# Performance work log

Hardware: AMD Instinct MI355X
Metric: run time of the kernel (lower is better)

Reference implementation:

```python
import jax, jax.numpy as jnp
import numpy as np
from jax import lax

H = 100  # hidden size hard-coded in the module


def setup_inputs() -> dict:
    key = jax.random.key(0)
    ks = jax.random.split(key, 13)
    T = 8192
    s = 1.0 / np.sqrt(H)  # torch LSTMCell/Linear init scale
    f32 = jnp.float32
    return {
        "input": jax.random.normal(ks[0], (T, 1), f32),
        "encoder_state_h": jax.random.normal(ks[1], (1, H), f32),
        "encoder_state_c": jax.random.normal(ks[2], (1, H), f32),
        "w_ih1": jax.random.normal(ks[3], (4 * H, 1), f32) * s,
        "w_hh1": jax.random.normal(ks[4], (4 * H, H), f32) * s,
        "b_ih1": jax.random.normal(ks[5], (4 * H,), f32) * s,
        "b_hh1": jax.random.normal(ks[6], (4 * H,), f32) * s,
        "w_ih2": jax.random.normal(ks[7], (4 * H, H), f32) * s,
        "w_hh2": jax.random.normal(ks[8], (4 * H, H), f32) * s,
        "b_ih2": jax.random.normal(ks[9], (4 * H,), f32) * s,
        "b_hh2": jax.random.normal(ks[10], (4 * H,), f32) * s,
        "w_lin": jax.random.normal(ks[11], (1, H), f32) * s,
        "b_lin": jax.random.normal(ks[12], (1,), f32) * s,
        "future": 1024,
    }


def _lstm_cell(x, h, c, w_ih, w_hh, b_ih, b_hh):
    # torch.nn.LSTMCell: gates ordered i, f, g, o
    gates = x @ w_ih.T + h @ w_hh.T + b_ih + b_hh  # (1, 4H)
    i, f, g, o = jnp.split(gates, 4, axis=-1)
    c_new = jax.nn.sigmoid(f) * c + jax.nn.sigmoid(i) * jnp.tanh(g)
    h_new = jax.nn.sigmoid(o) * jnp.tanh(c_new)
    return h_new, c_new


def reference(input, encoder_state_h, encoder_state_c,
              w_ih1, w_hh1, b_ih1, b_hh1,
              w_ih2, w_hh2, b_ih2, b_hh2,
              w_lin, b_lin, future):
    dt = input.dtype

    def step(carry, x_t):
        h1, c1, h2, c2 = carry
        h1, c1 = _lstm_cell(x_t, h1, c1, w_ih1, w_hh1, b_ih1, b_hh1)
        h2, c2 = _lstm_cell(h1, h2, c2, w_ih2, w_hh2, b_ih2, b_hh2)
        y = h2 @ w_lin.T + b_lin  # (1, 1)
        return (h1, c1, h2, c2), y

    carry0 = (encoder_state_h, encoder_state_c,
              jnp.zeros((1, H), dt), jnp.zeros((1, H), dt))
    xs = input[:, None, :]  # (T, 1, 1): per-step (1,1) input as in chunk(dim=0)
    carry, ys = lax.scan(step, carry0, xs)
    seq_out = ys[:, 0, 0][None, :]  # (1, T)

    if future:
        def fstep(carry, _):
            h1, c1, h2, c2, y = carry
            h1, c1 = _lstm_cell(y, h1, c1, w_ih1, w_hh1, b_ih1, b_hh1)
            h2, c2 = _lstm_cell(h1, h2, c2, w_ih2, w_hh2, b_ih2, b_hh2)
            y = h2 @ w_lin.T + b_lin
            return (h1, c1, h2, c2, y), y

        fcarry0 = carry + (ys[-1],)
        _, fys = lax.scan(fstep, fcarry0, None, length=future)
        fut_out = fys[:, 0, 0][None, :]  # (1, future)
        return jnp.concatenate([seq_out, fut_out], axis=1)  # (1, T+future)
    return seq_out
```

## Files before the change

### kernel.cpp

```cpp
#include <hip/hip_runtime.h>
#include <math.h>


#define HH 100
#define NT 512
#define ROWS 400
#define SPIN_CAP 2000000u

#define OFF_AW     0
#define OFF_P2W    128
#define OFF_BPROG  256
#define OFF_YPROG  384
#define OFF_YSLOT  512
#define OFF_RING   16384

#define VMCNT0() asm volatile("s_waitcnt vmcnt(0)" ::: "memory")
#define VMCNT2() asm volatile("s_waitcnt vmcnt(2)" ::: "memory")
#define LGKM0()  asm volatile("s_waitcnt lgkmcnt(0)" ::: "memory")
#define CLOB()   asm volatile("" ::: "memory")

__device__ __forceinline__ float rl(float v, int k) {
    return __int_as_float(__builtin_amdgcn_readlane(__float_as_int(v), k));
}
__device__ __forceinline__ unsigned san(unsigned v) { return v > 0x00FFFFFFu ? 0u : v; }
__device__ __forceinline__ unsigned ldu(const unsigned* p) {
    return san(__hip_atomic_load((unsigned*)p, __ATOMIC_RELAXED, __HIP_MEMORY_SCOPE_AGENT));
}
__device__ __forceinline__ void stu(unsigned* p, unsigned v) {
    __hip_atomic_store(p, v, __ATOMIC_RELAXED, __HIP_MEMORY_SCOPE_AGENT);
}
__device__ __forceinline__ float ld_f(const float* p) {
    return __hip_atomic_load((float*)p, __ATOMIC_RELAXED, __HIP_MEMORY_SCOPE_AGENT);
}
__device__ __forceinline__ void st_wt(float* p, float v) {
    __hip_atomic_store(p, v, __ATOMIC_RELAXED, __HIP_MEMORY_SCOPE_AGENT);
}
__device__ __forceinline__ void wait_ge(unsigned* p, unsigned need, unsigned& cache) {
    if (cache >= need) return;
    unsigned s = 0;
    do { cache = ldu(p); } while (cache < need && ++s < SPIN_CAP);
    VMCNT0();
}
__device__ __forceinline__ void wait_min8(unsigned* q, unsigned need, unsigned& cache) {
    if (cache >= need) return;
    unsigned s = 0;
    for (;;) {
        unsigned m0 = ldu(q), m1 = ldu(q + 1), m2 = ldu(q + 2), m3 = ldu(q + 3);
        unsigned m4 = ldu(q + 4), m5 = ldu(q + 5), m6 = ldu(q + 6), m7 = ldu(q + 7);
        unsigned a = m0 < m1 ? m0 : m1, b = m2 < m3 ? m2 : m3;
        unsigned c = m4 < m5 ? m4 : m5, d = m6 < m7 ? m6 : m7;
        a = a < b ? a : b;  c = c < d ? c : d;
        cache = a < c ? a : c;
        if (cache >= need || ++s > SPIN_CAP) break;
    }
    VMCNT0();
}
__device__ __forceinline__ void bar() {
    LGKM0();
    __builtin_amdgcn_s_barrier();
    CLOB();
}
__device__ __forceinline__ float fast_sigm(float x) {
    return __builtin_amdgcn_rcpf(1.0f + __expf(-x));
}
__device__ __forceinline__ float fast_tanh(float x) {
    return fmaf(-2.0f, __builtin_amdgcn_rcpf(1.0f + __expf(2.0f * x)), 1.0f);
}
__device__ __forceinline__ const float4* opqp(const float4* p) {
    unsigned long long u = (unsigned long long)p;
    asm("" : "+v"(u));
    return (const float4*)u;
}

#define REP25(M) M(0) M(1) M(2) M(3) M(4) M(5) M(6) M(7) M(8) M(9) M(10) M(11) \
                 M(12) M(13) M(14) M(15) M(16) M(17) M(18) M(19) M(20) M(21) M(22) M(23) M(24)
#define DECLW(i) float4 W_##i;
#define LOADW(i) W_##i = wrow[i];
#define DOTC(i) { \
    const float hsv = ((i) < 16) ? hv0 : hv1; \
    const int kb = ((i) < 16) ? (4 * (i)) : (4 * ((i) - 16)); \
    float h0 = rl(hsv, kb), h1 = rl(hsv, kb + 1), h2 = rl(hsv, kb + 2), h3 = rl(hsv, kb + 3); \
    a0 = fmaf(W_##i.x, h0, a0); a1 = fmaf(W_##i.y, h1, a1); \
    a0 = fmaf(W_##i.z, h2, a0); a1 = fmaf(W_##i.w, h3, a1); \
}

extern "C" __global__ void __launch_bounds__(NT, 2)
__attribute__((amdgpu_waves_per_eu(2, 2)))
decoder_kernel(const float* __restrict__ input,
               const float* __restrict__ enc_h,
               const float* __restrict__ enc_c,
               const float* __restrict__ w_ih1,
               const float* __restrict__ w_hh1,
               const float* __restrict__ b_ih1,
               const float* __restrict__ b_hh1,
               const float* __restrict__ w_ih2,
               const float* __restrict__ w_hh2,
               const float* __restrict__ b_ih2,
               const float* __restrict__ b_hh2,
               const float* __restrict__ w_lin,
               const float* __restrict__ b_lin,
               float* __restrict__ out,
               char* __restrict__ ws,
               int T, int F, int S)
{
    const int tid = threadIdx.x;
    const int l = tid & 63;
    const int w = tid >> 6;
    unsigned* aw     = (unsigned*)(ws + OFF_AW);
    unsigned* p2w    = (unsigned*)(ws + OFF_P2W);
    unsigned* b_prog = (unsigned*)(ws + OFF_BPROG);
    unsigned* y_prog = (unsigned*)(ws + OFF_YPROG);
    float* y_slot = (float*)(ws + OFF_YSLOT);
    float* ring1  = (float*)(ws + OFF_RING);
    float* ring2  = ring1 + (size_t)S * HH;
    const int smask = S - 1;
    const int TOT = T + F;

    const int cell = 16 * w + (l & 15);
    const int gate = l >> 4;
    const bool valid = (cell < 100);
    const bool c_lane = (gate == 0) && valid;

    if (blockIdx.x == 0) {
        __shared__ __align__(16) float h1s[2][128];
        const int j = valid ? (cell + 100 * gate) : 0;
        const float4* wrow = opqp((const float4*)(w_hh1 + (size_t)j * HH));
        REP25(DECLW)
        REP25(LOADW)
        const float wx = w_ih1[j];
        const float bi = b_ih1[j] + b_hh1[j];
        float cst = c_lane ? enc_c[cell] : 0.f;
        if (tid < 128) {
            h1s[0][tid] = (tid < HH) ? enc_h[tid] : 0.f;
            h1s[1][tid] = 0.f;
        }
        __syncthreads();

        unsigned cp2 = 0, cy = 0;
        for (int t = 0; t < TOT; ++t) {
            VMCNT0();
            if (l == 0 && t > 0) stu(&aw[w], (unsigned)t);
            float x = 0.f;
            if (t < T) x = input[t];
            if (t >= S) wait_min8(p2w, (unsigned)(t - S + 1), cp2);
            float hv0 = h1s[t & 1][l];
            float hv1 = h1s[t & 1][64 + l];
            float a0 = 0.f, a1 = 0.f;
            REP25(DOTC)
            float acc = bi + a0 + a1;
            if (t >= T) {
                wait_ge(y_prog, (unsigned)(t - T + 1), cy);
                x = ld_f(&y_slot[t - T]);
            }
            acc = fmaf(x, wx, acc);
            float v = (gate == 2) ? fast_tanh(acc) : fast_sigm(acc);
            float gf = __shfl(v, (l & 15) + 16);
            float gg = __shfl(v, (l & 15) + 32);
            float go = __shfl(v, (l & 15) + 48);
            if (c_lane) {
                cst = fmaf(gf, cst, v * gg);
                float h = go * fast_tanh(cst);
                h1s[(t + 1) & 1][cell] = h;
                st_wt(&ring1[(size_t)(t & smask) * HH + cell], h);
            }
            bar();
        }
        VMCNT0();
        if (l == 0) stu(&aw[w], (unsigned)TOT);
    } else if (blockIdx.x == 1) {
        const bool av = (tid < ROWS);
        const int j = av ? tid : 0;
        const float4* wrow = opqp((const float4*)(w_ih2 + (size_t)j * HH));
        REP25(DECLW)
        REP25(LOADW)
        const float bi = b_ih2[j] + b_hh2[j];

        unsigned ca = 0, cb = 0;
        wait_min8(aw, 1u, ca);
        float cv0 = ld_f(ring1 + l);
        float cv1 = (l < 36) ? ld_f(ring1 + 64 + l) : 0.f;
        for (int t = 1; t < T; ++t) {
            VMCNT2();
            if (l == 0 && t >= 3) stu(&p2w[w], (unsigned)(t - 2));
            if (t - 1 >= S) wait_ge(b_prog, (unsigned)(t - S), cb);
            wait_min8(aw, (unsigned)(t + 1), ca);
            const float* rp = ring1 + (size_t)(t & smask) * HH;
            float nv0 = ld_f(rp + l);
            float nv1 = (l < 36) ? ld_f(rp + 64 + l) : 0.f;
            float hv0 = cv0, hv1 = cv1;
            float a0 = 0.f, a1 = 0.f;
            REP25(DOTC)
            float* wpp = ring2 + (size_t)((t - 1) & smask) * ROWS;
            if (av) st_wt(wpp + j, bi + a0 + a1);
            cv0 = nv0; cv1 = nv1;
        }
        VMCNT0();
        if (l == 0) stu(&p2w[w], (unsigned)(T - 1));
        {
            if (T - 1 >= S) wait_ge(b_prog, (unsigned)(T - S), cb);
            float hv0 = cv0, hv1 = cv1;
            float a0 = 0.f, a1 = 0.f;
            REP25(DOTC)
            float* wpp = ring2 + (size_t)((T - 1) & smask) * ROWS;
            if (av) st_wt(wpp + j, bi + a0 + a1);
        }
        VMCNT0();
        if (l == 0) stu(&p2w[w], (unsigned)T);
        for (int t = T; t < TOT; ++t) {
            if (t >= S) wait_ge(b_prog, (unsigned)(t - S + 1), cb);
            wait_min8(aw, (unsigned)(t + 1), ca);
            const float* rp = ring1 + (size_t)(t & smask) * HH;
            float hv0 = ld_f(rp + l);
            float hv1 = (l < 36) ? ld_f(rp + 64 + l) : 0.f;
            float a0 = 0.f, a1 = 0.f;
            REP25(DOTC)
            float* wpp = ring2 + (size_t)(t & smask) * ROWS;
            if (av) st_wt(wpp + j, bi + a0 + a1);
            VMCNT0();
            if (l == 0) stu(&p2w[w], (unsigned)(t + 1));
        }
    } else {
        __shared__ __align__(16) float h2s[2][128];
        __shared__ float yw[2][8];
        const int j = valid ? (cell + 100 * gate) : 0;
        const float4* wrow = opqp((const float4*)(w_hh2 + (size_t)j * HH));
        REP25(DECLW)
        REP25(LOADW)
        const float wl = c_lane ? w_lin[cell] : 0.f;
        const float bl = b_lin[0];
        float cst = 0.f;
        if (tid < 128) { h2s[0][tid] = 0.f; h2s[1][tid] = 0.f; }
        __syncthreads();

        unsigned cpB = 0;
        for (int u = 0; u < TOT; ++u) {
            if (tid == 0 && u > 0) {
                const float* yq = yw[(u - 1) & 1];
                float y = yq[0] + yq[1] + yq[2] + yq[3] + yq[4] + yq[5] + yq[6] + bl;
                stu(b_prog, (unsigned)u);
                if (u - 1 >= T - 1) {
                    st_wt(&y_slot[(u - 1) - (T - 1)], y);
                    VMCNT0();
                    stu(y_prog, (unsigned)(u - T + 1));
                }
                out[u - 1] = y;
            }
            float hv0 = h2s[u & 1][l];
            float hv1 = h2s[u & 1][64 + l];
            const float* pp = ring2 + (size_t)(u & smask) * ROWS;
            float pre;
            float a0 = 0.f, a1 = 0.f;
            if (u < T) {
                wait_min8(p2w, (unsigned)(u + 1), cpB);
                pre = ld_f(pp + j);
                REP25(DOTC)
            } else {
                REP25(DOTC)
                wait_min8(p2w, (unsigned)(u + 1), cpB);
                pre = ld_f(pp + j);
            }
            float acc = pre + a0 + a1;
            float v = (gate == 2) ? fast_tanh(acc) : fast_sigm(acc);
            float gf = __shfl(v, (l & 15) + 16);
            float gg = __shfl(v, (l & 15) + 32);
            float go = __shfl(v, (l & 15) + 48);
            float py = 0.f;
            if (c_lane) {
                cst = fmaf(gf, cst, v * gg);
                float h = go * fast_tanh(cst);
                h2s[(u + 1) & 1][cell] = h;
                py = h * wl;
            }
            py += __shfl_down(py, 8);
            py += __shfl_down(py, 4);
            py += __shfl_down(py, 2);
            py += __shfl_down(py, 1);
            if (l == 0 && w < 7) yw[u & 1][w] = py;
            bar();
        }
        if (tid == 0) {
            const float* yq = yw[(TOT - 1) & 1];
            out[TOT - 1] = yq[0] + yq[1] + yq[2] + yq[3] + yq[4] + yq[5] + yq[6] + bl;
        }
    }
}

extern "C" void kernel_launch(void* const* d_in, const int* in_sizes, int n_in,
                              void* d_out, int out_size, void* d_ws, size_t ws_size,
                              hipStream_t stream) {
    const float* input = (const float*)d_in[0];
    const float* enc_h = (const float*)d_in[1];
    const float* enc_c = (const float*)d_in[2];
    const float* w_ih1 = (const float*)d_in[3];
    const float* w_hh1 = (const float*)d_in[4];
    const float* b_ih1 = (const float*)d_in[5];
    const float* b_hh1 = (const float*)d_in[6];
    const float* w_ih2 = (const float*)d_in[7];
    const float* w_hh2 = (const float*)d_in[8];
    const float* b_ih2 = (const float*)d_in[9];
    const float* b_hh2 = (const float*)d_in[10];
    const float* w_lin = (const float*)d_in[11];
    const float* b_lin = (const float*)d_in[12];
    (void)n_in;

    int T = in_sizes[0];
    int F = out_size - T;
    if (F < 0) F = 0;

    int S = 16;
    while ((size_t)OFF_RING + (size_t)S * 2 * (HH + ROWS) * 4 <= ws_size && S < 8192)
        S <<= 1;

    decoder_kernel<<<dim3(3), dim3(NT), 0, stream>>>(
        input, enc_h, enc_c, w_ih1, w_hh1, b_ih1, b_hh1,
        w_ih2, w_hh2, b_ih2, b_hh2, w_lin, b_lin,
        (float*)d_out, (char*)d_ws, T, F, S);
}
```

Baseline: 16.83 ms.

## Move recurrent weights from registers to LDS plus per-step global reads

Recurrent weights were held in registers. Each block now stages the first 36 columns of its weight matrix into dynamic shared memory at startup and reads the remaining 64 columns from global memory on every timestep. The register-pinning asm trick and the waves-per-EU hint are removed. This lowers register pressure, but it puts LDS and global (L1/L2) loads on the serial recurrence's critical path every step.

After: 29.87 ms. 1.78x slower.

```diff
diff --git a/kernel.cpp b/kernel.cpp
--- a/kernel.cpp
+++ b/kernel.cpp
@@ -5,6 +5,8 @@
 #define HH 100
 #define NT 512
 #define ROWS 400
+#define LCH 9
+#define LDW (LCH * 4)
 #define SPIN_CAP 2000000u
 
 #define OFF_AW     0
@@ -18,6 +20,8 @@
 #define VMCNT2() asm volatile("s_waitcnt vmcnt(2)" ::: "memory")
 #define LGKM0()  asm volatile("s_waitcnt lgkmcnt(0)" ::: "memory")
 #define CLOB()   asm volatile("" ::: "memory")
+
+extern __shared__ __attribute__((aligned(16))) float ldsW[];
 
 __device__ __forceinline__ float rl(float v, int k) {
     return __int_as_float(__builtin_amdgcn_readlane(__float_as_int(v), k));
@@ -66,26 +70,23 @@
 __device__ __forceinline__ float fast_tanh(float x) {
     return fmaf(-2.0f, __builtin_amdgcn_rcpf(1.0f + __expf(2.0f * x)), 1.0f);
 }
-__device__ __forceinline__ const float4* opqp(const float4* p) {
-    unsigned long long u = (unsigned long long)p;
-    asm("" : "+v"(u));
-    return (const float4*)u;
-}
-
-#define REP25(M) M(0) M(1) M(2) M(3) M(4) M(5) M(6) M(7) M(8) M(9) M(10) M(11) \
-                 M(12) M(13) M(14) M(15) M(16) M(17) M(18) M(19) M(20) M(21) M(22) M(23) M(24)
-#define DECLW(i) float4 W_##i;
-#define LOADW(i) W_##i = wrow[i];
-#define DOTC(i) { \
+
+#define DOTS(i, P) { \
     const float hsv = ((i) < 16) ? hv0 : hv1; \
     const int kb = ((i) < 16) ? (4 * (i)) : (4 * ((i) - 16)); \
+    float4 Wc = P[(i) < LCH ? (i) : ((i) - 0)]; \
     float h0 = rl(hsv, kb), h1 = rl(hsv, kb + 1), h2 = rl(hsv, kb + 2), h3 = rl(hsv, kb + 3); \
-    a0 = fmaf(W_##i.x, h0, a0); a1 = fmaf(W_##i.y, h1, a1); \
-    a0 = fmaf(W_##i.z, h2, a0); a1 = fmaf(W_##i.w, h3, a1); \
-}
-
-extern "C" __global__ void __launch_bounds__(NT, 2)
-__attribute__((amdgpu_waves_per_eu(2, 2)))
+    a0 = fmaf(Wc.x, h0, a0); a1 = fmaf(Wc.y, h1, a1); \
+    a0 = fmaf(Wc.z, h2, a0); a1 = fmaf(Wc.w, h3, a1); \
+}
+#define DOTL(i) DOTS(i, lrow)
+#define DOTG(i) DOTS(i, grow)
+#define REP9L(M)  M(0) M(1) M(2) M(3) M(4) M(5) M(6) M(7) M(8)
+#define REP16G(M) M(9) M(10) M(11) M(12) M(13) M(14) M(15) M(16) \
+                  M(17) M(18) M(19) M(20) M(21) M(22) M(23) M(24)
+#define DOT_FULL() { REP16G(DOTG) REP9L(DOTL) }
+
+extern "C" __global__ void __launch_bounds__(NT)
 decoder_kernel(const float* __restrict__ input,
                const float* __restrict__ enc_h,
                const float* __restrict__ enc_c,
@@ -121,12 +122,21 @@
     const bool valid = (cell < 100);
     const bool c_lane = (gate == 0) && valid;
 
+    {
+        const float* wsrc = (blockIdx.x == 0) ? w_hh1
+                          : (blockIdx.x == 1) ? w_ih2 : w_hh2;
+        const int n = ROWS * LDW;
+        for (int i = tid; i < n; i += NT) {
+            int r = i / LDW, c = i - r * LDW;
+            ldsW[i] = wsrc[r * HH + c];
+        }
+    }
+
     if (blockIdx.x == 0) {
         __shared__ __align__(16) float h1s[2][128];
         const int j = valid ? (cell + 100 * gate) : 0;
-        const float4* wrow = opqp((const float4*)(w_hh1 + (size_t)j * HH));
-        REP25(DECLW)
-        REP25(LOADW)
+        const float4* lrow = (const float4*)(ldsW + (size_t)j * LDW);
+        const float4* grow = (const float4*)(w_hh1 + (size_t)j * HH);
         const float wx = w_ih1[j];
         const float bi = b_ih1[j] + b_hh1[j];
         float cst = c_lane ? enc_c[cell] : 0.f;
@@ -146,7 +156,7 @@
             float hv0 = h1s[t & 1][l];
             float hv1 = h1s[t & 1][64 + l];
             float a0 = 0.f, a1 = 0.f;
-            REP25(DOTC)
+            DOT_FULL()
             float acc = bi + a0 + a1;
             if (t >= T) {
                 wait_ge(y_prog, (unsigned)(t - T + 1), cy);
@@ -170,10 +180,10 @@
     } else if (blockIdx.x == 1) {
         const bool av = (tid < ROWS);
         const int j = av ? tid : 0;
-        const float4* wrow = opqp((const float4*)(w_ih2 + (size_t)j * HH));
-        REP25(DECLW)
-        REP25(LOADW)
+        const float4* lrow = (const float4*)(ldsW + (size_t)j * LDW);
+        const float4* grow = (const float4*)(w_ih2 + (size_t)j * HH);
         const float bi = b_ih2[j] + b_hh2[j];
+        __syncthreads();
 
         unsigned ca = 0, cb = 0;
         wait_min8(aw, 1u, ca);
@@ -189,7 +199,7 @@
             float nv1 = (l < 36) ? ld_f(rp + 64 + l) : 0.f;
             float hv0 = cv0, hv1 = cv1;
             float a0 = 0.f, a1 = 0.f;
-            REP25(DOTC)
+            DOT_FULL()
             float* wpp = ring2 + (size_t)((t - 1) & smask) * ROWS;
             if (av) st_wt(wpp + j, bi + a0 + a1);
             cv0 = nv0; cv1 = nv1;
@@ -200,7 +210,7 @@
             if (T - 1 >= S) wait_ge(b_prog, (unsigned)(T - S), cb);
             float hv0 = cv0, hv1 = cv1;
             float a0 = 0.f, a1 = 0.f;
-            REP25(DOTC)
+            DOT_FULL()
             float* wpp = ring2 + (size_t)((T - 1) & smask) * ROWS;
             if (av) st_wt(wpp + j, bi + a0 + a1);
         }
@@ -213,7 +223,7 @@
             float hv0 = ld_f(rp + l);
             float hv1 = (l < 36) ? ld_f(rp + 64 + l) : 0.f;
             float a0 = 0.f, a1 = 0.f;
-            REP25(DOTC)
+            DOT_FULL()
             float* wpp = ring2 + (size_t)(t & smask) * ROWS;
             if (av) st_wt(wpp + j, bi + a0 + a1);
             VMCNT0();
@@ -223,9 +233,8 @@
         __shared__ __align__(16) float h2s[2][128];
         __shared__ float yw[2][8];
         const int j = valid ? (cell + 100 * gate) : 0;
-        const float4* wrow = opqp((const float4*)(w_hh2 + (size_t)j * HH));
-        REP25(DECLW)
-        REP25(LOADW)
+        const float4* lrow = (const float4*)(ldsW + (size_t)j * LDW);
+        const float4* grow = (const float4*)(w_hh2 + (size_t)j * HH);
         const float wl = c_lane ? w_lin[cell] : 0.f;
         const float bl = b_lin[0];
         float cst = 0.f;
@@ -253,9 +262,9 @@
             if (u < T) {
                 wait_min8(p2w, (unsigned)(u + 1), cpB);
                 pre = ld_f(pp + j);
-                REP25(DOTC)
+                DOT_FULL()
             } else {
-                REP25(DOTC)
+                DOT_FULL()
                 wait_min8(p2w, (unsigned)(u + 1), cpB);
                 pre = ld_f(pp + j);
             }
@@ -311,7 +320,9 @@
     while ((size_t)OFF_RING + (size_t)S * 2 * (HH + ROWS) * 4 <= ws_size && S < 8192)
         S <<= 1;
 
-    decoder_kernel<<<dim3(3), dim3(NT), 0, stream>>>(
+    const size_t dyn = (size_t)ROWS * LDW * sizeof(float);
+
+    decoder_kernel<<<dim3(3), dim3(NT), dyn, stream>>>(
         input, enc_h, enc_c, w_ih1, w_hh1, b_ih1, b_hh1,
         w_ih2, w_hh2, b_ih2, b_hh2, w_lin, b_lin,
         (float*)d_out, (char*)d_ws, T, F, S);
```

## Split each LSTM stage across two blocks with per-step cross-block state exchange

Applied to the files above, without the earlier changes.

Each recurrent stage (layer-1 recurrence, layer-2 input projection, layer-2 recurrence) now runs on two blocks of 256 threads instead of one block of 512, each owning about half the hidden cells. Every step, each half publishes its new h values and a progress counter to global memory and reads the peer's half, so the full hidden vector can be rebuilt. The output y is split into two partial sums that are combined later with a lag. Weights are re-read from memory each step instead of being held in registers. The aim is shorter per-step compute, but it adds a global-memory round trip and peer synchronisation to every step of the serial recurrence.

Result: slower. 31.76 ms (+88.7%).

```diff
diff --git a/kernel.cpp b/kernel.cpp
--- a/kernel.cpp
+++ b/kernel.cpp
@@ -3,16 +3,25 @@
 
 
 #define HH 100
-#define NT 512
-#define ROWS 400
+#define NT 256
 #define SPIN_CAP 2000000u
-
-#define OFF_AW     0
-#define OFF_P2W    128
-#define OFF_BPROG  256
-#define OFF_YPROG  384
-#define OFF_YSLOT  512
-#define OFF_RING   16384
+#define LAG 64
+
+#define OFF_AW0   0
+#define OFF_AW1   128
+#define OFF_P2A   256
+#define OFF_P2B   384
+#define OFF_B0P   512
+#define OFF_B1P   640
+#define OFF_BY0   768
+#define OFF_BY1   896
+#define OFF_BW0   1024
+#define OFF_BW1   1152
+#define OFF_Y0ALL 4096
+#define OFF_Y1ALL 40960
+#define OFF_H2RA  77824
+#define OFF_H2RB  80896
+#define OFF_RING  98304
 
 #define VMCNT0() asm volatile("s_waitcnt vmcnt(0)" ::: "memory")
 #define VMCNT2() asm volatile("s_waitcnt vmcnt(2)" ::: "memory")
@@ -41,16 +50,13 @@
     do { cache = ldu(p); } while (cache < need && ++s < SPIN_CAP);
     VMCNT0();
 }
-__device__ __forceinline__ void wait_min8(unsigned* q, unsigned need, unsigned& cache) {
+__device__ __forceinline__ void wait_min4(unsigned* q, unsigned need, unsigned& cache) {
     if (cache >= need) return;
     unsigned s = 0;
     for (;;) {
         unsigned m0 = ldu(q), m1 = ldu(q + 1), m2 = ldu(q + 2), m3 = ldu(q + 3);
-        unsigned m4 = ldu(q + 4), m5 = ldu(q + 5), m6 = ldu(q + 6), m7 = ldu(q + 7);
         unsigned a = m0 < m1 ? m0 : m1, b = m2 < m3 ? m2 : m3;
-        unsigned c = m4 < m5 ? m4 : m5, d = m6 < m7 ? m6 : m7;
-        a = a < b ? a : b;  c = c < d ? c : d;
-        cache = a < c ? a : c;
+        cache = a < b ? a : b;
         if (cache >= need || ++s > SPIN_CAP) break;
     }
     VMCNT0();
@@ -66,26 +72,19 @@
 __device__ __forceinline__ float fast_tanh(float x) {
     return fmaf(-2.0f, __builtin_amdgcn_rcpf(1.0f + __expf(2.0f * x)), 1.0f);
 }
-__device__ __forceinline__ const float4* opqp(const float4* p) {
-    unsigned long long u = (unsigned long long)p;
-    asm("" : "+v"(u));
-    return (const float4*)u;
-}
 
 #define REP25(M) M(0) M(1) M(2) M(3) M(4) M(5) M(6) M(7) M(8) M(9) M(10) M(11) \
                  M(12) M(13) M(14) M(15) M(16) M(17) M(18) M(19) M(20) M(21) M(22) M(23) M(24)
-#define DECLW(i) float4 W_##i;
-#define LOADW(i) W_##i = wrow[i];
 #define DOTC(i) { \
     const float hsv = ((i) < 16) ? hv0 : hv1; \
     const int kb = ((i) < 16) ? (4 * (i)) : (4 * ((i) - 16)); \
+    float4 Wc = grow[i]; \
     float h0 = rl(hsv, kb), h1 = rl(hsv, kb + 1), h2 = rl(hsv, kb + 2), h3 = rl(hsv, kb + 3); \
-    a0 = fmaf(W_##i.x, h0, a0); a1 = fmaf(W_##i.y, h1, a1); \
-    a0 = fmaf(W_##i.z, h2, a0); a1 = fmaf(W_##i.w, h3, a1); \
-}
-
-extern "C" __global__ void __launch_bounds__(NT, 2)
-__attribute__((amdgpu_waves_per_eu(2, 2)))
+    a0 = fmaf(Wc.x, h0, a0); a1 = fmaf(Wc.y, h1, a1); \
+    a0 = fmaf(Wc.z, h2, a0); a1 = fmaf(Wc.w, h3, a1); \
+}
+
+extern "C" __global__ void __launch_bounds__(NT, 1)
 decoder_kernel(const float* __restrict__ input,
                const float* __restrict__ enc_h,
                const float* __restrict__ enc_c,
@@ -106,181 +105,267 @@
     const int tid = threadIdx.x;
     const int l = tid & 63;
     const int w = tid >> 6;
-    unsigned* aw     = (unsigned*)(ws + OFF_AW);
-    unsigned* p2w    = (unsigned*)(ws + OFF_P2W);
-    unsigned* b_prog = (unsigned*)(ws + OFF_BPROG);
-    unsigned* y_prog = (unsigned*)(ws + OFF_YPROG);
-    float* y_slot = (float*)(ws + OFF_YSLOT);
-    float* ring1  = (float*)(ws + OFF_RING);
-    float* ring2  = ring1 + (size_t)S * HH;
+    const int m = l & 15;
+    float* ring1a = (float*)(ws + OFF_RING);
+    float* ring1b = ring1a + (size_t)S * 48;
+    float* ring2a = ring1b + (size_t)S * 52;
+    float* ring2b = ring2a + (size_t)S * 192;
+    float* y0all = (float*)(ws + OFF_Y0ALL);
+    float* y1all = (float*)(ws + OFF_Y1ALL);
+    unsigned* p2a = (unsigned*)(ws + OFF_P2A);
+    unsigned* p2b = (unsigned*)(ws + OFF_P2B);
     const int smask = S - 1;
     const int TOT = T + F;
-
-    const int cell = 16 * w + (l & 15);
-    const int gate = l >> 4;
-    const bool valid = (cell < 100);
-    const bool c_lane = (gate == 0) && valid;
-
-    if (blockIdx.x == 0) {
-        __shared__ __align__(16) float h1s[2][128];
+    const int bid = blockIdx.x;
+
+    if (bid < 2) {
+        const int half = bid;
+        const int cbase = half ? 48 : 0;
+        const int ccnt  = half ? 52 : 48;
+        const int myW   = ccnt;
+        const int peerW = half ? 48 : 52;
+        float* myRing   = half ? ring1b : ring1a;
+        float* peerRing = half ? ring1a : ring1b;
+        unsigned* myAw   = (unsigned*)(ws + (half ? OFF_AW1 : OFF_AW0));
+        unsigned* peerAw = (unsigned*)(ws + (half ? OFF_AW0 : OFF_AW1));
+        unsigned* by0 = (unsigned*)(ws + OFF_BY0);
+        unsigned* by1 = (unsigned*)(ws + OFF_BY1);
+
+        __shared__ __align__(16) float h1s[2][64];
+        const int local = 16 * w + m;
+        const bool valid = local < ccnt;
+        const int cell = cbase + (valid ? local : 0);
+        const int gate = l >> 4;
+        const bool c_lane = (gate == 0) && valid;
         const int j = valid ? (cell + 100 * gate) : 0;
-        const float4* wrow = opqp((const float4*)(w_hh1 + (size_t)j * HH));
-        REP25(DECLW)
-        REP25(LOADW)
+        const float4* grow = (const float4*)(w_hh1 + (size_t)j * HH);
         const float wx = w_ih1[j];
         const float bi = b_ih1[j] + b_hh1[j];
         float cst = c_lane ? enc_c[cell] : 0.f;
-        if (tid < 128) {
-            h1s[0][tid] = (tid < HH) ? enc_h[tid] : 0.f;
-            h1s[1][tid] = 0.f;
-        }
+        if (tid < 64) { h1s[0][tid] = 0.f; h1s[1][tid] = 0.f; }
         __syncthreads();
 
-        unsigned cp2 = 0, cy = 0;
+        unsigned cg1 = 0, cg2 = 0, cpeer = 0, cy0 = 0, cy1 = 0;
         for (int t = 0; t < TOT; ++t) {
             VMCNT0();
-            if (l == 0 && t > 0) stu(&aw[w], (unsigned)t);
+            if (l == 0 && t > 0) stu(&myAw[w], (unsigned)t);
             float x = 0.f;
             if (t < T) x = input[t];
-            if (t >= S) wait_min8(p2w, (unsigned)(t - S + 1), cp2);
-            float hv0 = h1s[t & 1][l];
-            float hv1 = h1s[t & 1][64 + l];
+            if (t >= S) { wait_min4(p2a, (unsigned)(t - S + 1), cg1);
+                          wait_min4(p2b, (unsigned)(t - S + 1), cg2); }
+            float hv0, hv1;
+            if (t == 0) {
+                hv0 = enc_h[l];
+                hv1 = (l < 36) ? enc_h[64 + l] : 0.f;
+            } else {
+                wait_min4(peerAw, (unsigned)t, cpeer);
+                const float* pr = peerRing + (size_t)((t - 1) & smask) * peerW;
+                if (half == 0) {
+                    hv0 = (l < 48) ? h1s[t & 1][l] : ld_f(pr + (l - 48));
+                    hv1 = (l < 36) ? ld_f(pr + (16 + l)) : 0.f;
+                } else {
+                    hv0 = (l < 48) ? ld_f(pr + l) : h1s[t & 1][l - 48];
+                    hv1 = (l < 36) ? h1s[t & 1][16 + l] : 0.f;
+                }
+            }
             float a0 = 0.f, a1 = 0.f;
             REP25(DOTC)
             float acc = bi + a0 + a1;
             if (t >= T) {
-                wait_ge(y_prog, (unsigned)(t - T + 1), cy);
-                x = ld_f(&y_slot[t - T]);
+                wait_ge(by0, (unsigned)(t - T + 1), cy0);
+                wait_ge(by1, (unsigned)(t - T + 1), cy1);
+                x = ld_f(y0all + (t - 1)) + ld_f(y1all + (t - 1));
             }
             acc = fmaf(x, wx, acc);
             float v = (gate == 2) ? fast_tanh(acc) : fast_sigm(acc);
-            float gf = __shfl(v, (l & 15) + 16);
-            float gg = __shfl(v, (l & 15) + 32);
-            float go = __shfl(v, (l & 15) + 48);
+            float gf = __shfl(v, m + 16);
+            float gg = __shfl(v, m + 32);
+            float go = __shfl(v, m + 48);
             if (c_lane) {
                 cst = fmaf(gf, cst, v * gg);
                 float h = go * fast_tanh(cst);
-                h1s[(t + 1) & 1][cell] = h;
-                st_wt(&ring1[(size_t)(t & smask) * HH + cell], h);
+                h1s[(t + 1) & 1][local] = h;
+                st_wt(myRing + (size_t)(t & smask) * myW + local, h);
             }
             bar();
         }
         VMCNT0();
-        if (l == 0) stu(&aw[w], (unsigned)TOT);
-    } else if (blockIdx.x == 1) {
-        const bool av = (tid < ROWS);
-        const int j = av ? tid : 0;
-        const float4* wrow = opqp((const float4*)(w_ih2 + (size_t)j * HH));
-        REP25(DECLW)
-        REP25(LOADW)
+        if (l == 0) stu(&myAw[w], (unsigned)TOT);
+    } else if (bid < 4) {
+        const int half = bid - 2;
+        const int ccnt = half ? 52 : 48;
+        const int cbase = half ? 48 : 0;
+        const bool valid = l < ccnt;
+        const int gate = w;
+        const int cell = cbase + (valid ? l : 0);
+        const int j = valid ? (cell + 100 * gate) : 0;
+        const int oidx = (valid ? l : 0) + ccnt * gate;
+        float* myR2 = half ? ring2b : ring2a;
+        const int r2W = half ? 208 : 192;
+        unsigned* myP2  = (unsigned*)(ws + (half ? OFF_P2B : OFF_P2A));
+        unsigned* bprog = (unsigned*)(ws + (half ? OFF_B1P : OFF_B0P));
+        unsigned* aw0 = (unsigned*)(ws + OFF_AW0);
+        unsigned* aw1 = (unsigned*)(ws + OFF_AW1);
+        const float4* grow = (const float4*)(w_ih2 + (size_t)j * HH);
         const float bi = b_ih2[j] + b_hh2[j];
 
-        unsigned ca = 0, cb = 0;
-        wait_min8(aw, 1u, ca);
-        float cv0 = ld_f(ring1 + l);
-        float cv1 = (l < 36) ? ld_f(ring1 + 64 + l) : 0.f;
+        unsigned ca0 = 0, ca1 = 0, cb = 0;
+        wait_min4(aw0, 1u, ca0);
+        wait_min4(aw1, 1u, ca1);
+        float cv0 = (l < 48) ? ld_f(ring1a + l) : ld_f(ring1b + (l - 48));
+        float cv1 = (l < 36) ? ld_f(ring1b + (16 + l)) : 0.f;
         for (int t = 1; t < T; ++t) {
             VMCNT2();
-            if (l == 0 && t >= 3) stu(&p2w[w], (unsigned)(t - 2));
-            if (t - 1 >= S) wait_ge(b_prog, (unsigned)(t - S), cb);
-            wait_min8(aw, (unsigned)(t + 1), ca);
-            const float* rp = ring1 + (size_t)(t & smask) * HH;
-            float nv0 = ld_f(rp + l);
-            float nv1 = (l < 36) ? ld_f(rp + 64 + l) : 0.f;
+            if (l == 0 && t >= 3) stu(&myP2[w], (unsigned)(t - 2));
+            if (t - 1 >= S) wait_ge(bprog, (unsigned)(t - S), cb);
+            wait_min4(aw0, (unsigned)(t + 1), ca0);
+            wait_min4(aw1, (unsigned)(t + 1), ca1);
+            const float* ra = ring1a + (size_t)(t & smask) * 48;
+            const float* rb = ring1b + (size_t)(t & smask) * 52;
+            float nv0 = (l < 48) ? ld_f(ra + l) : ld_f(rb + (l - 48));
+            float nv1 = (l < 36) ? ld_f(rb + (16 + l)) : 0.f;
             float hv0 = cv0, hv1 = cv1;
             float a0 = 0.f, a1 = 0.f;
             REP25(DOTC)
-            float* wpp = ring2 + (size_t)((t - 1) & smask) * ROWS;
-            if (av) st_wt(wpp + j, bi + a0 + a1);
+            float* wp = myR2 + (size_t)((t - 1) & smask) * r2W;
+            if (valid) st_wt(wp + oidx, bi + a0 + a1);
             cv0 = nv0; cv1 = nv1;
         }
         VMCNT0();
-        if (l == 0) stu(&p2w[w], (unsigned)(T - 1));
+        if (l == 0) stu(&myP2[w], (unsigned)(T - 1));
         {
-            if (T - 1 >= S) wait_ge(b_prog, (unsigned)(T - S), cb);
+            if (T - 1 >= S) wait_ge(bprog, (unsigned)(T - S), cb);
             float hv0 = cv0, hv1 = cv1;
             float a0 = 0.f, a1 = 0.f;
             REP25(DOTC)
-            float* wpp = ring2 + (size_t)((T - 1) & smask) * ROWS;
-            if (av) st_wt(wpp + j, bi + a0 + a1);
+            float* wp = myR2 + (size_t)((T - 1) & smask) * r2W;
+            if (valid) st_wt(wp + oidx, bi + a0 + a1);
         }
         VMCNT0();
-        if (l == 0) stu(&p2w[w], (unsigned)T);
+        if (l == 0) stu(&myP2[w], (unsigned)T);
         for (int t = T; t < TOT; ++t) {
-            if (t >= S) wait_ge(b_prog, (unsigned)(t - S + 1), cb);
-            wait_min8(aw, (unsigned)(t + 1), ca);
-            const float* rp = ring1 + (size_t)(t & smask) * HH;
-            float hv0 = ld_f(rp + l);
-            float hv1 = (l < 36) ? ld_f(rp + 64 + l) : 0.f;
+            if (t >= S) wait_ge(bprog, (unsigned)(t - S + 1), cb);
+            wait_min4(aw0, (unsigned)(t + 1), ca0);
+            wait_min4(aw1, (unsigned)(t + 1), ca1);
+            const float* ra = ring1a + (size_t)(t & smask) * 48;
+            const float* rb = ring1b + (size_t)(t & smask) * 52;
+            float hv0 = (l < 48) ? ld_f(ra + l) : ld_f(rb + (l - 48));
+            float hv1 = (l < 36) ? ld_f(rb + (16 + l)) : 0.f;
             float a0 = 0.f, a1 = 0.f;
             REP25(DOTC)
-            float* wpp = ring2 + (size_t)(t & smask) * ROWS;
-            if (av) st_wt(wpp + j, bi + a0 + a1);
+            float* wp = myR2 + (size_t)(t & smask) * r2W;
+            if (valid) st_wt(wp + oidx, bi + a0 + a1);
             VMCNT0();
-            if (l == 0) stu(&p2w[w], (unsigned)(t + 1));
+            if (l == 0) stu(&myP2[w], (unsigned)(t + 1));
         }
     } else {
-        __shared__ __align__(16) float h2s[2][128];
-        __shared__ float yw[2][8];
+        const int half = bid - 4;
+        const int cbase = half ? 48 : 0;
+        const int ccnt = half ? 52 : 48;
+        const int myW = ccnt, peerW = half ? 48 : 52;
+        float* myH2R   = (float*)(ws + (half ? OFF_H2RB : OFF_H2RA));
+        float* peerH2R = (float*)(ws + (half ? OFF_H2RA : OFF_H2RB));
+        unsigned* myBw   = (unsigned*)(ws + (half ? OFF_BW1 : OFF_BW0));
+        unsigned* peerBw = (unsigned*)(ws + (half ? OFF_BW0 : OFF_BW1));
+        unsigned* myBp = (unsigned*)(ws + (half ? OFF_B1P : OFF_B0P));
+        unsigned* myBy = (unsigned*)(ws + (half ? OFF_BY1 : OFF_BY0));
+        unsigned* b1p  = (unsigned*)(ws + OFF_B1P);
+        float* myYall = half ? y1all : y0all;
+        float* myR2 = half ? ring2b : ring2a;
+        const int r2W = half ? 208 : 192;
+        unsigned* p2h = (unsigned*)(ws + (half ? OFF_P2B : OFF_P2A));
+
+        __shared__ __align__(16) float h2s[2][64];
+        __shared__ float yw[2][4];
+        const int local = 16 * w + m;
+        const bool valid = local < ccnt;
+        const int cell = cbase + (valid ? local : 0);
+        const int gate = l >> 4;
+        const bool c_lane = (gate == 0) && valid;
         const int j = valid ? (cell + 100 * gate) : 0;
-        const float4* wrow = opqp((const float4*)(w_hh2 + (size_t)j * HH));
-        REP25(DECLW)
-        REP25(LOADW)
+        const int pidx = (valid ? local : 0) + ccnt * gate;
+        const float4* grow = (const float4*)(w_hh2 + (size_t)j * HH);
         const float wl = c_lane ? w_lin[cell] : 0.f;
-        const float bl = b_lin[0];
+        const float bl = half ? 0.f : b_lin[0];
         float cst = 0.f;
-        if (tid < 128) { h2s[0][tid] = 0.f; h2s[1][tid] = 0.f; }
+        if (tid < 64) { h2s[0][tid] = 0.f; h2s[1][tid] = 0.f; }
+        if (tid < 8) yw[tid >> 2][tid & 3] = 0.f;
         __syncthreads();
 
-        unsigned cpB = 0;
+        unsigned cp = 0, cpe = 0, cb1g = 0;
         for (int u = 0; u < TOT; ++u) {
+            VMCNT0();
+            if (l == 0 && u > 0) stu(&myBw[w], (unsigned)u);
             if (tid == 0 && u > 0) {
+                stu(myBp, (unsigned)u);
                 const float* yq = yw[(u - 1) & 1];
-                float y = yq[0] + yq[1] + yq[2] + yq[3] + yq[4] + yq[5] + yq[6] + bl;
-                stu(b_prog, (unsigned)u);
-                if (u - 1 >= T - 1) {
-                    st_wt(&y_slot[(u - 1) - (T - 1)], y);
-                    VMCNT0();
-                    stu(y_prog, (unsigned)(u - T + 1));
+                float yp = yq[0] + yq[1] + yq[2] + yq[3] + bl;
+                st_wt(&myYall[u - 1], yp);
+                if (u >= T) { VMCNT0(); stu(myBy, (unsigned)(u - T + 1)); }
+                if (half == 0 && u - 1 >= LAG) {
+                    int v = u - 1 - LAG;
+                    wait_ge(b1p, (unsigned)(v + 2), cb1g);
+                    out[v] = ld_f(y0all + v) + ld_f(y1all + v);
                 }
-                out[u - 1] = y;
-            }
-            float hv0 = h2s[u & 1][l];
-            float hv1 = h2s[u & 1][64 + l];
-            const float* pp = ring2 + (size_t)(u & smask) * ROWS;
-            float pre;
+            }
+            float hv0, hv1;
+            if (u == 0) { hv0 = 0.f; hv1 = 0.f; }
+            else {
+                wait_min4(peerBw, (unsigned)u, cpe);
+                const float* pr = peerH2R + (size_t)((u - 1) & 15) * peerW;
+                if (half == 0) {
+                    hv0 = (l < 48) ? h2s[u & 1][l] : ld_f(pr + (l - 48));
+                    hv1 = (l < 36) ? ld_f(pr + (16 + l)) : 0.f;
+                } else {
+                    hv0 = (l < 48) ? ld_f(pr + l) : h2s[u & 1][l - 48];
+                    hv1 = (l < 36) ? h2s[u & 1][16 + l] : 0.f;
+                }
+            }
+            float pre = 0.f;
             float a0 = 0.f, a1 = 0.f;
             if (u < T) {
-                wait_min8(p2w, (unsigned)(u + 1), cpB);
-                pre = ld_f(pp + j);
+                wait_min4(p2h, (unsigned)(u + 1), cp);
+                const float* pp = myR2 + (size_t)(u & smask) * r2W;
+                pre = ld_f(pp + pidx);
                 REP25(DOTC)
             } else {
                 REP25(DOTC)
-                wait_min8(p2w, (unsigned)(u + 1), cpB);
-                pre = ld_f(pp + j);
+                wait_min4(p2h, (unsigned)(u + 1), cp);
+                const float* pp = myR2 + (size_t)(u & smask) * r2W;
+                pre = ld_f(pp + pidx);
             }
             float acc = pre + a0 + a1;
             float v = (gate == 2) ? fast_tanh(acc) : fast_sigm(acc);
-            float gf = __shfl(v, (l & 15) + 16);
-            float gg = __shfl(v, (l & 15) + 32);
-            float go = __shfl(v, (l & 15) + 48);
+            float gf = __shfl(v, m + 16);
+            float gg = __shfl(v, m + 32);
+            float go = __shfl(v, m + 48);
             float py = 0.f;
             if (c_lane) {
                 cst = fmaf(gf, cst, v * gg);
                 float h = go * fast_tanh(cst);
-                h2s[(u + 1) & 1][cell] = h;
+                h2s[(u + 1) & 1][local] = h;
+                st_wt(myH2R + (size_t)(u & 15) * myW + local, h);
                 py = h * wl;
             }
             py += __shfl_down(py, 8);
             py += __shfl_down(py, 4);
             py += __shfl_down(py, 2);
             py += __shfl_down(py, 1);
-            if (l == 0 && w < 7) yw[u & 1][w] = py;
+            if (l == 0) yw[u & 1][w] = py;
             bar();
         }
         if (tid == 0) {
             const float* yq = yw[(TOT - 1) & 1];
-            out[TOT - 1] = yq[0] + yq[1] + yq[2] + yq[3] + yq[4] + yq[5] + yq[6] + bl;
+            float yp = yq[0] + yq[1] + yq[2] + yq[3] + bl;
+            st_wt(&myYall[TOT - 1], yp);
+            VMCNT0();
+            stu(myBp, (unsigned)(TOT + 2));
+            if (half == 0) {
+                unsigned cfin = 0;
+                wait_ge(b1p, (unsigned)(TOT + 2), cfin);
+                for (int v2 = TOT - 1 - LAG; v2 < TOT; ++v2)
+                    out[v2] = ld_f(y0all + v2) + ld_f(y1all + v2);
+            }
         }
     }
 }
@@ -308,10 +393,10 @@
     if (F < 0) F = 0;
 
     int S = 16;
-    while ((size_t)OFF_RING + (size_t)S * 2 * (HH + ROWS) * 4 <= ws_size && S < 8192)
+    while ((size_t)OFF_RING + (size_t)S * 4000 <= ws_size && S < 8192)
         S <<= 1;
 
-    decoder_kernel<<<dim3(3), dim3(NT), 0, stream>>>(
+    decoder_kernel<<<dim3(6), dim3(NT), 0, stream>>>(
         input, enc_h, enc_c, w_ih1, w_hh1, b_ih1, b_hh1,
         w_ih2, w_hh2, b_ih2, b_hh2, w_lin, b_lin,
         (float*)d_out, (char*)d_ws, T, F, S);
```
